# Kernel optimization log

Measured on AMD Instinct MI355X. Metric: run time of the kernel, lower is better.

Reference implementation:

```python
import jax, jax.numpy as jnp
import numpy as np

B, N, D, K = 16, 512, 64, 8  # batch, num_nodes, node_dim, num_edge_class


def setup_inputs() -> dict:
    key = jax.random.key(0)
    ks = jax.random.split(key, 6)
    return {
        "node_states": jax.random.normal(ks[0], (B, N, D), jnp.float32),
        "adjacency_in": jax.random.randint(ks[1], (B, N, N), 0, K + 1, jnp.int32),
        "distance": jax.random.normal(ks[2], (B, N, N), jnp.float32),  # declared but unused, as in source
        "matrices_in": jax.random.normal(ks[3], (K, D, D), jnp.float32) * 0.1,
        "matrices_out": jax.random.normal(ks[4], (K, D, D), jnp.float32) * 0.1,
        "message_bias": jax.random.normal(ks[5], (2 * D,), jnp.float32) * 0.1,
    }


def reference(node_states, adjacency_in, distance, matrices_in, matrices_out, message_bias):
    # node_states: [B, N, D]; adjacency_in: [B, N, N] int in [0, K]; 0 = no edge.
    node_dim = node_states.shape[-1]
    zeros = jnp.zeros((1, node_dim, node_dim), node_states.dtype)
    Min = jnp.concatenate([zeros, matrices_in], axis=0)    # [K+1, D, D]
    Mout = jnp.concatenate([zeros, matrices_out], axis=0)  # [K+1, D, D]
    # Transform every node state by every edge-type matrix once:
    # T[b, j, k, d] = sum_e M[k, d, e] * h[b, j, e]
    T_in = jnp.einsum('kde,bje->bjkd', Min, node_states)
    T_out = jnp.einsum('kde,bje->bjkd', Mout, node_states)
    # One-hot edge types: oh[b, i, j, k] = [adjacency_in[b, i, j] == k]
    oh = jax.nn.one_hot(adjacency_in, Min.shape[0], dtype=node_states.dtype)  # [B, N, N, K+1]
    # a_in_mul[b, i, d]  = sum_j M_in[adj[b,i,j]]  @ h[b, j]  (identical math to the
    # dense [B, N*D, N*D] block-matmul in the TF source, without materializing it)
    a_in_mul = jnp.einsum('bijk,bjkd->bid', oh, T_in)
    # a_out uses the transposed adjacency: adj_out[b,i,j] = adj[b,j,i]
    a_out_mul = jnp.einsum('bjik,bjkd->bid', oh, T_out)
    messages = jnp.concatenate([a_in_mul, a_out_mul], axis=-1) + message_bias
    return messages  # [B, N, 2*D]
```

## Files before the change

### kernel.cpp

```cpp
#include <hip/hip_runtime.h>
#include <hip/hip_fp16.h>

#define B_ 16
#define N_ 512
#define D_ 64
#define K_ 8

#define WSU_BYTES ((size_t)B_ * N_ * N_ * 4)
#define T_BYTES   ((size_t)B_ * N_ * (K_ + 1) * D_ * 2)
#define HBF_BYTES ((size_t)B_ * N_ * D_ * 2)
#define MBF_BYTES ((size_t)2 * K_ * D_ * D_ * 2)
#define TROWB 1152

typedef __attribute__((ext_vector_type(8))) short bf8_t;
typedef __attribute__((ext_vector_type(4))) float f4_t;

__device__ __forceinline__ unsigned short f2bf(float x) {
  union { float f; unsigned u; } c; c.f = x;
  unsigned r = c.u + 0x7FFFu + ((c.u >> 16) & 1u);
  return (unsigned short)(r >> 16);
}

__global__ __launch_bounds__(256) void conv_inputs(
    const float* __restrict__ h, const float* __restrict__ Min,
    const float* __restrict__ Mout,
    unsigned short* __restrict__ hbf, unsigned short* __restrict__ Mbf,
    unsigned short* __restrict__ Tin, unsigned short* __restrict__ Tout) {
  const int g = blockIdx.x * 256 + threadIdx.x;
  {
    const float4 v = ((const float4*)h)[g];
    ushort4 o; o.x = f2bf(v.x); o.y = f2bf(v.y); o.z = f2bf(v.z); o.w = f2bf(v.w);
    ((ushort4*)hbf)[g] = o;
  }
  if (g < 8192) {
    const float4 v = ((const float4*)Min)[g];
    ushort4 o; o.x = f2bf(v.x); o.y = f2bf(v.y); o.z = f2bf(v.z); o.w = f2bf(v.w);
    ((ushort4*)Mbf)[g] = o;
  } else if (g < 16384) {
    const int t = g - 8192;
    const float4 v = ((const float4*)Mout)[t];
    ushort4 o; o.x = f2bf(v.x); o.y = f2bf(v.y); o.z = f2bf(v.z); o.w = f2bf(v.w);
    ((ushort4*)Mbf)[8192 + t] = o;
  }
  {
    const int row = g >> 4, part = g & 15;
    const ushort4 z = make_ushort4(0, 0, 0, 0);
    ((ushort4*)(Tin  + (size_t)row * 576))[part] = z;
    ((ushort4*)(Tout + (size_t)row * 576))[part] = z;
  }
}

__global__ __launch_bounds__(256) void prep_adj(const int* __restrict__ adj,
                                                unsigned* __restrict__ wsu) {
  __shared__ int ta[64][65];
  __shared__ int tb[64][65];
  const int blk = blockIdx.x;
  const int xcd = blk & 7, rest = blk >> 3;
  const int b = xcd + 8 * (rest & 1);
  const int tile = rest >> 1;
  const int i0 = (tile >> 3) * 64, j0 = (tile & 7) * 64;
  const int lane = threadIdx.x & 63, w = threadIdx.x >> 6;
  const int* ab = adj + (size_t)b * N_ * N_;
#pragma unroll
  for (int r = w; r < 64; r += 4) {
    ta[r][lane] = ab[(size_t)(i0 + r) * N_ + j0 + lane];
    tb[r][lane] = ab[(size_t)(j0 + r) * N_ + i0 + lane];
  }
  __syncthreads();
  unsigned* wb = wsu + (size_t)b * N_ * N_;
#pragma unroll
  for (int r = w; r < 64; r += 4) {
    wb[(size_t)(i0 + r) * N_ + j0 + lane] =
        (unsigned)(ta[r][lane] << 7) | ((unsigned)tb[lane][r] << 23);
  }
}

__global__ __launch_bounds__(256) void build_T_mfma(
    const unsigned short* __restrict__ hbf,
    const unsigned short* __restrict__ Mbf,
    unsigned short* __restrict__ Tin,
    unsigned short* __restrict__ Tout) {
  const int blk = blockIdx.x;
  const int b   = (blk & 7) + 8 * ((blk >> 3) & 1);
  const int u   = blk >> 4;
  const int kdt = u >> 3;
  const int jt4 = u & 7;
  const int w = threadIdx.x >> 6, l = threadIdx.x & 63;
  const int j0  = (jt4 * 4 + w) * 16;
  const int kd0 = kdt * 64;
  const int r16 = l & 15, grp = l >> 4;

  const unsigned short* hr = hbf + ((size_t)(b * N_ + j0 + r16)) * 64 + grp * 8;
  bf8_t hfr[2];
  hfr[0] = *(const bf8_t*)(hr);
  hfr[1] = *(const bf8_t*)(hr + 32);

  const unsigned short* mr = Mbf + (size_t)(kd0 + r16) * 64 + grp * 8;

  f4_t acc[4];
#pragma unroll
  for (int fc = 0; fc < 4; ++fc) acc[fc] = (f4_t)(0.f);
#pragma unroll
  for (int fc = 0; fc < 4; ++fc) {
    const bf8_t a0 = *(const bf8_t*)(mr + (size_t)fc * 16 * 64);
    const bf8_t a1 = *(const bf8_t*)(mr + (size_t)fc * 16 * 64 + 32);
    acc[fc] = __builtin_amdgcn_mfma_f32_16x16x32_bf16(a0, hfr[0], acc[fc], 0, 0, 0);
    acc[fc] = __builtin_amdgcn_mfma_f32_16x16x32_bf16(a1, hfr[1], acc[fc], 0, 0, 0);
  }

  unsigned short* Tb = ((kd0 & 512) ? Tout : Tin) + (size_t)b * N_ * 576;
  const int kdl = kd0 & 511;
  const int j = j0 + r16;
  unsigned short* trow = Tb + (size_t)j * 576 + 64 + kdl + grp * 4;
#pragma unroll
  for (int fc = 0; fc < 4; ++fc) {
    const __half2 lo = __floats2half2_rn(acc[fc][0], acc[fc][1]);
    const __half2 hi = __floats2half2_rn(acc[fc][2], acc[fc][3]);
    uint2 pk;
    pk.x = *(const unsigned*)&lo;
    pk.y = *(const unsigned*)&hi;
    *(uint2*)(trow + fc * 16) = pk;
  }
}

__global__ __launch_bounds__(512) void gather_msg(
    const unsigned* __restrict__ wsu,
    const unsigned short* __restrict__ Tin,
    const float* __restrict__ bias,
    float* __restrict__ out) {
  __shared__ unsigned ed[16][512];
  const int blk = blockIdx.x;
  const int b  = (blk & 7) + 8 * ((blk >> 3) & 1);
  const int rb = blk >> 4;
  const int tid = threadIdx.x;
  const int w = tid >> 6, lane = tid & 63;
  const int half = lane >> 5, lane5 = lane & 31;
  const int dir = lane5 >> 4;
  const int dl  = lane5 & 15;
  const int row_l = w * 2 + half;

  {
    const int4* src = (const int4*)(wsu + ((size_t)(b * N_ + rb * 16)) * N_);
    int4* dst = (int4*)ed;
#pragma unroll
    for (int c = 0; c < 4; ++c) dst[c * 512 + tid] = src[c * 512 + tid];
  }
  __syncthreads();

  const unsigned shr_ = (unsigned)dir * 16u;
  const char* base = (const char*)Tin + (size_t)b * N_ * TROWB;
  unsigned vb = (unsigned)dir * (unsigned)T_BYTES + (unsigned)dl * 8u;
  const unsigned* edrow = &ed[row_l][0];

  float fa0 = 0.f, fa1 = 0.f, fa2 = 0.f, fa3 = 0.f;
  for (int jw = 0; jw < 8; ++jw) {
    __half2 a0 = __floats2half2_rn(0.f, 0.f);
    __half2 a1 = __floats2half2_rn(0.f, 0.f);
#pragma unroll 4
    for (int j4 = 0; j4 < 16; ++j4) {
      const uint4 ew = *(const uint4*)(edrow + jw * 64 + j4 * 4);
#pragma unroll
      for (int t = 0; t < 4; ++t) {
        const unsigned wvv = (t == 0) ? ew.x : (t == 1) ? ew.y : (t == 2) ? ew.z : ew.w;
        const unsigned off = (wvv >> shr_) & 0xFFFFu;
        const uint2 u = *(const uint2*)(base + (vb + off));
        a0 = __hadd2(a0, *(const __half2*)&u.x);
        a1 = __hadd2(a1, *(const __half2*)&u.y);
        vb += TROWB;
      }
    }
    const float2 f0 = __half22float2(a0);
    const float2 f1 = __half22float2(a1);
    fa0 += f0.x; fa1 += f0.y; fa2 += f1.x; fa3 += f1.y;
  }

  const int row = rb * 16 + row_l;
  const int d0 = dl * 4;
  float4 r;
  r.x = fa0 + bias[dir * 64 + d0];
  r.y = fa1 + bias[dir * 64 + d0 + 1];
  r.z = fa2 + bias[dir * 64 + d0 + 2];
  r.w = fa3 + bias[dir * 64 + d0 + 3];
  *(float4*)(out + ((size_t)b * N_ + row) * (2 * D_) + dir * 64 + d0) = r;
}

#define ACCUM(kv, bucket) switch (kv) { \
    case 1: (bucket)[0] += v_; break; case 2: (bucket)[1] += v_; break; \
    case 3: (bucket)[2] += v_; break; case 4: (bucket)[3] += v_; break; \
    case 5: (bucket)[4] += v_; break; case 6: (bucket)[5] += v_; break; \
    case 7: (bucket)[6] += v_; break; case 8: (bucket)[7] += v_; break; \
    default: break; }

__global__ __launch_bounds__(64) void ggnn_fallback(
    const float* __restrict__ h, const int* __restrict__ adj,
    const float* __restrict__ Min, const float* __restrict__ Mout,
    const float* __restrict__ bias, float* __restrict__ out) {
  const int blk = blockIdx.x;
  const int b  = blk / (N_ / 2);
  const int i0 = (blk % (N_ / 2)) * 2;
  const int d  = threadIdx.x;
  float s_in[2][K_], s_out[2][K_];
#pragma unroll
  for (int r = 0; r < 2; ++r)
#pragma unroll
    for (int k = 0; k < K_; ++k) { s_in[r][k] = 0.f; s_out[r][k] = 0.f; }
  const int* rowp0 = adj + (b * N_ + i0) * N_;
  const int* rowp1 = rowp0 + N_;
  const int* colp  = adj + b * N_ * N_ + i0;
  const float* hb  = h + b * N_ * D_ + d;
  for (int j0 = 0; j0 < N_; j0 += 8) {
    float hv[8]; int kr0[8], kr1[8], kc0[8], kc1[8];
#pragma unroll
    for (int m = 0; m < 8; ++m) {
      hv[m] = hb[(j0 + m) * D_];
      kr0[m] = rowp0[j0 + m]; kr1[m] = rowp1[j0 + m];
      kc0[m] = colp[(j0 + m) * N_]; kc1[m] = colp[(j0 + m) * N_ + 1];
    }
#pragma unroll
    for (int m = 0; m < 8; ++m) {
      const float v_ = hv[m];
      ACCUM(kr0[m], s_in[0]); ACCUM(kr1[m], s_in[1]);
      ACCUM(kc0[m], s_out[0]); ACCUM(kc1[m], s_out[1]);
    }
  }
  __shared__ float S[2][2][K_][D_];
#pragma unroll
  for (int r = 0; r < 2; ++r)
#pragma unroll
    for (int k = 0; k < K_; ++k) { S[r][0][k][d] = s_in[r][k]; S[r][1][k][d] = s_out[r][k]; }
  __syncthreads();
  float acc_in[2], acc_out[2];
#pragma unroll
  for (int r = 0; r < 2; ++r) { acc_in[r] = bias[d]; acc_out[r] = bias[D_ + d]; }
  for (int k = 0; k < K_; ++k) {
#pragma unroll
    for (int e0 = 0; e0 < D_; e0 += 4) {
      const float4 mi = *(const float4*)(Min  + (k * D_ + d) * D_ + e0);
      const float4 mo = *(const float4*)(Mout + (k * D_ + d) * D_ + e0);
#pragma unroll
      for (int r = 0; r < 2; ++r) {
        const float4 si = *(const float4*)(&S[r][0][k][e0]);
        const float4 so = *(const float4*)(&S[r][1][k][e0]);
        acc_in[r]  += mi.x * si.x + mi.y * si.y + mi.z * si.z + mi.w * si.w;
        acc_out[r] += mo.x * so.x + mo.y * so.y + mo.z * so.z + mo.w * so.w;
      }
    }
  }
#pragma unroll
  for (int r = 0; r < 2; ++r) {
    out[(b * N_ + i0 + r) * (2 * D_) + d]      = acc_in[r];
    out[(b * N_ + i0 + r) * (2 * D_) + D_ + d] = acc_out[r];
  }
}

extern "C" void kernel_launch(void* const* d_in, const int* in_sizes, int n_in,
                              void* d_out, int out_size, void* d_ws, size_t ws_size,
                              hipStream_t stream) {
  const float* h    = (const float*)d_in[0];
  const int*   adj  = (const int*)d_in[1];
  const float* Min  = (const float*)d_in[3];
  const float* Mout = (const float*)d_in[4];
  const float* bias = (const float*)d_in[5];
  float* out = (float*)d_out;

  if (ws_size < WSU_BYTES + 2 * T_BYTES + HBF_BYTES + MBF_BYTES) {
    hipLaunchKernelGGL(ggnn_fallback, dim3(B_ * N_ / 2), dim3(64), 0, stream,
                       h, adj, Min, Mout, bias, out);
    return;
  }
  unsigned*       wsu  = (unsigned*)d_ws;
  unsigned short* Tin  = (unsigned short*)((char*)d_ws + WSU_BYTES);
  unsigned short* Tout = (unsigned short*)((char*)d_ws + WSU_BYTES + T_BYTES);
  unsigned short* hbf  = (unsigned short*)((char*)d_ws + WSU_BYTES + 2 * T_BYTES);
  unsigned short* Mbf  = (unsigned short*)((char*)d_ws + WSU_BYTES + 2 * T_BYTES + HBF_BYTES);

  hipLaunchKernelGGL(conv_inputs,  dim3(512),  dim3(256), 0, stream,
                     h, Min, Mout, hbf, Mbf, Tin, Tout);
  hipLaunchKernelGGL(prep_adj,     dim3(1024), dim3(256), 0, stream, adj, wsu);
  hipLaunchKernelGGL(build_T_mfma, dim3(2048), dim3(256), 0, stream, hbf, Mbf, Tin, Tout);
  hipLaunchKernelGGL(gather_msg,   dim3(512),  dim3(512), 0, stream,
                     wsu, Tin, bias, out);
}
```

Before: 166.2 us.

## Fold bf16 input conversion into T build and split gather over j halves

Removes the separate conv_inputs kernel. build_T_mfma now converts fp32 h and M to bf16 in registers, and its kdt==0 blocks zero the k=0 slots of T_in and T_out. gather_msg now handles 8 rows per block instead of 16. The block's two wave groups each cover half of the j range, and their partial sums are combined through shared memory. This doubles the grid to 1024 blocks and fully unrolls the inner loop, so more of the GPU stays busy and one launch plus one global pass disappear. The cost is repeated fp32-to-bf16 conversion of M across many blocks and an extra shared-memory reduction with syncs.

```diff
diff --git a/kernel.cpp b/kernel.cpp
--- a/kernel.cpp
+++ b/kernel.cpp
@@ -8,9 +8,8 @@
 
 #define WSU_BYTES ((size_t)B_ * N_ * N_ * 4)
 #define T_BYTES   ((size_t)B_ * N_ * (K_ + 1) * D_ * 2)
-#define HBF_BYTES ((size_t)B_ * N_ * D_ * 2)
-#define MBF_BYTES ((size_t)2 * K_ * D_ * D_ * 2)
 #define TROWB 1152
+#define TOUT_OFF (T_BYTES / 2)
 
 typedef __attribute__((ext_vector_type(8))) short bf8_t;
 typedef __attribute__((ext_vector_type(4))) float f4_t;
@@ -21,33 +20,15 @@
   return (unsigned short)(r >> 16);
 }
 
-__global__ __launch_bounds__(256) void conv_inputs(
-    const float* __restrict__ h, const float* __restrict__ Min,
-    const float* __restrict__ Mout,
-    unsigned short* __restrict__ hbf, unsigned short* __restrict__ Mbf,
-    unsigned short* __restrict__ Tin, unsigned short* __restrict__ Tout) {
-  const int g = blockIdx.x * 256 + threadIdx.x;
-  {
-    const float4 v = ((const float4*)h)[g];
-    ushort4 o; o.x = f2bf(v.x); o.y = f2bf(v.y); o.z = f2bf(v.z); o.w = f2bf(v.w);
-    ((ushort4*)hbf)[g] = o;
-  }
-  if (g < 8192) {
-    const float4 v = ((const float4*)Min)[g];
-    ushort4 o; o.x = f2bf(v.x); o.y = f2bf(v.y); o.z = f2bf(v.z); o.w = f2bf(v.w);
-    ((ushort4*)Mbf)[g] = o;
-  } else if (g < 16384) {
-    const int t = g - 8192;
-    const float4 v = ((const float4*)Mout)[t];
-    ushort4 o; o.x = f2bf(v.x); o.y = f2bf(v.y); o.z = f2bf(v.z); o.w = f2bf(v.w);
-    ((ushort4*)Mbf)[8192 + t] = o;
-  }
-  {
-    const int row = g >> 4, part = g & 15;
-    const ushort4 z = make_ushort4(0, 0, 0, 0);
-    ((ushort4*)(Tin  + (size_t)row * 576))[part] = z;
-    ((ushort4*)(Tout + (size_t)row * 576))[part] = z;
-  }
+__device__ __forceinline__ bf8_t pack_bf8(const float* p) {
+  const float4 a = *(const float4*)p;
+  const float4 b = *(const float4*)(p + 4);
+  union { unsigned u[4]; bf8_t v; } r;
+  r.u[0] = (unsigned)f2bf(a.x) | ((unsigned)f2bf(a.y) << 16);
+  r.u[1] = (unsigned)f2bf(a.z) | ((unsigned)f2bf(a.w) << 16);
+  r.u[2] = (unsigned)f2bf(b.x) | ((unsigned)f2bf(b.y) << 16);
+  r.u[3] = (unsigned)f2bf(b.z) | ((unsigned)f2bf(b.w) << 16);
+  return r.v;
 }
 
 __global__ __launch_bounds__(256) void prep_adj(const int* __restrict__ adj,
@@ -76,10 +57,10 @@
 }
 
 __global__ __launch_bounds__(256) void build_T_mfma(
-    const unsigned short* __restrict__ hbf,
-    const unsigned short* __restrict__ Mbf,
-    unsigned short* __restrict__ Tin,
-    unsigned short* __restrict__ Tout) {
+    const float* __restrict__ h,
+    const float* __restrict__ Min,
+    const float* __restrict__ Mout,
+    unsigned short* __restrict__ Tin) {
   const int blk = blockIdx.x;
   const int b   = (blk & 7) + 8 * ((blk >> 3) & 1);
   const int u   = blk >> 4;
@@ -90,25 +71,26 @@
   const int kd0 = kdt * 64;
   const int r16 = l & 15, grp = l >> 4;
 
-  const unsigned short* hr = hbf + ((size_t)(b * N_ + j0 + r16)) * 64 + grp * 8;
+  const float* hrp = h + ((size_t)(b * N_ + j0 + r16)) * 64 + grp * 8;
   bf8_t hfr[2];
-  hfr[0] = *(const bf8_t*)(hr);
-  hfr[1] = *(const bf8_t*)(hr + 32);
-
-  const unsigned short* mr = Mbf + (size_t)(kd0 + r16) * 64 + grp * 8;
+  hfr[0] = pack_bf8(hrp);
+  hfr[1] = pack_bf8(hrp + 32);
+
+  const float* Mbase = (kd0 >= 512) ? Mout : Min;
+  const float* mrp = Mbase + (size_t)((kd0 & 511) + r16) * 64 + grp * 8;
 
   f4_t acc[4];
 #pragma unroll
   for (int fc = 0; fc < 4; ++fc) acc[fc] = (f4_t)(0.f);
 #pragma unroll
   for (int fc = 0; fc < 4; ++fc) {
-    const bf8_t a0 = *(const bf8_t*)(mr + (size_t)fc * 16 * 64);
-    const bf8_t a1 = *(const bf8_t*)(mr + (size_t)fc * 16 * 64 + 32);
+    const bf8_t a0 = pack_bf8(mrp + (size_t)fc * 16 * 64);
+    const bf8_t a1 = pack_bf8(mrp + (size_t)fc * 16 * 64 + 32);
     acc[fc] = __builtin_amdgcn_mfma_f32_16x16x32_bf16(a0, hfr[0], acc[fc], 0, 0, 0);
     acc[fc] = __builtin_amdgcn_mfma_f32_16x16x32_bf16(a1, hfr[1], acc[fc], 0, 0, 0);
   }
 
-  unsigned short* Tb = ((kd0 & 512) ? Tout : Tin) + (size_t)b * N_ * 576;
+  unsigned short* Tb = Tin + ((kd0 >= 512) ? TOUT_OFF : 0) + (size_t)b * N_ * 576;
   const int kdl = kd0 & 511;
   const int j = j0 + r16;
   unsigned short* trow = Tb + (size_t)j * 576 + 64 + kdl + grp * 4;
@@ -121,42 +103,53 @@
     pk.y = *(const unsigned*)&hi;
     *(uint2*)(trow + fc * 16) = pk;
   }
-}
-
-__global__ __launch_bounds__(512) void gather_msg(
+
+  if (kdt == 0) {
+    unsigned short* s0 = Tin + (size_t)b * N_ * 576 + (size_t)j * 576 + grp * 16;
+    const int4 z = make_int4(0, 0, 0, 0);
+    *(int4*)(s0)                 = z;
+    *(int4*)(s0 + 8)             = z;
+    *(int4*)(s0 + TOUT_OFF)      = z;
+    *(int4*)(s0 + TOUT_OFF + 8)  = z;
+  }
+}
+
+__global__ __launch_bounds__(512, 8) void gather_msg(
     const unsigned* __restrict__ wsu,
     const unsigned short* __restrict__ Tin,
     const float* __restrict__ bias,
     float* __restrict__ out) {
-  __shared__ unsigned ed[16][512];
+  __shared__ unsigned ed[8 * 512];
   const int blk = blockIdx.x;
   const int b  = (blk & 7) + 8 * ((blk >> 3) & 1);
   const int rb = blk >> 4;
   const int tid = threadIdx.x;
   const int w = tid >> 6, lane = tid & 63;
+  const int wq = w & 3, jh = w >> 2;
   const int half = lane >> 5, lane5 = lane & 31;
   const int dir = lane5 >> 4;
   const int dl  = lane5 & 15;
-  const int row_l = w * 2 + half;
+  const int row_l = wq * 2 + half;
 
   {
-    const int4* src = (const int4*)(wsu + ((size_t)(b * N_ + rb * 16)) * N_);
+    const int4* src = (const int4*)(wsu + ((size_t)(b * N_ + rb * 8)) * N_);
     int4* dst = (int4*)ed;
-#pragma unroll
-    for (int c = 0; c < 4; ++c) dst[c * 512 + tid] = src[c * 512 + tid];
-  }
-  __syncthreads();
-
+    dst[tid]       = src[tid];
+    dst[tid + 512] = src[tid + 512];
+  }
+  __syncthreads();
+
+  const unsigned* edrow = ed + row_l * 512 + jh * 256;
   const unsigned shr_ = (unsigned)dir * 16u;
   const char* base = (const char*)Tin + (size_t)b * N_ * TROWB;
-  unsigned vb = (unsigned)dir * (unsigned)T_BYTES + (unsigned)dl * 8u;
-  const unsigned* edrow = &ed[row_l][0];
+  unsigned vb = (unsigned)jh * 256u * (unsigned)TROWB +
+                (unsigned)dir * (unsigned)T_BYTES + (unsigned)dl * 8u;
 
   float fa0 = 0.f, fa1 = 0.f, fa2 = 0.f, fa3 = 0.f;
-  for (int jw = 0; jw < 8; ++jw) {
+  for (int jw = 0; jw < 4; ++jw) {
     __half2 a0 = __floats2half2_rn(0.f, 0.f);
     __half2 a1 = __floats2half2_rn(0.f, 0.f);
-#pragma unroll 4
+#pragma unroll
     for (int j4 = 0; j4 < 16; ++j4) {
       const uint4 ew = *(const uint4*)(edrow + jw * 64 + j4 * 4);
 #pragma unroll
@@ -174,14 +167,21 @@
     fa0 += f0.x; fa1 += f0.y; fa2 += f1.x; fa3 += f1.y;
   }
 
-  const int row = rb * 16 + row_l;
-  const int d0 = dl * 4;
-  float4 r;
-  r.x = fa0 + bias[dir * 64 + d0];
-  r.y = fa1 + bias[dir * 64 + d0 + 1];
-  r.z = fa2 + bias[dir * 64 + d0 + 2];
-  r.w = fa3 + bias[dir * 64 + d0 + 3];
-  *(float4*)(out + ((size_t)b * N_ + row) * (2 * D_) + dir * 64 + d0) = r;
+  __syncthreads();
+  float4* pbuf = (float4*)ed;
+  if (jh == 1) pbuf[wq * 64 + lane] = make_float4(fa0, fa1, fa2, fa3);
+  __syncthreads();
+  if (jh == 0) {
+    const float4 p = pbuf[wq * 64 + lane];
+    const int row = rb * 8 + row_l;
+    const int d0 = dl * 4;
+    float4 r;
+    r.x = fa0 + p.x + bias[dir * 64 + d0];
+    r.y = fa1 + p.y + bias[dir * 64 + d0 + 1];
+    r.z = fa2 + p.z + bias[dir * 64 + d0 + 2];
+    r.w = fa3 + p.w + bias[dir * 64 + d0 + 3];
+    *(float4*)(out + ((size_t)b * N_ + row) * (2 * D_) + dir * 64 + d0) = r;
+  }
 }
 
 #define ACCUM(kv, bucket) switch (kv) { \
@@ -263,21 +263,15 @@
   const float* bias = (const float*)d_in[5];
   float* out = (float*)d_out;
 
-  if (ws_size < WSU_BYTES + 2 * T_BYTES + HBF_BYTES + MBF_BYTES) {
+  if (ws_size < WSU_BYTES + 2 * T_BYTES) {
     hipLaunchKernelGGL(ggnn_fallback, dim3(B_ * N_ / 2), dim3(64), 0, stream,
                        h, adj, Min, Mout, bias, out);
     return;
   }
-  unsigned*       wsu  = (unsigned*)d_ws;
-  unsigned short* Tin  = (unsigned short*)((char*)d_ws + WSU_BYTES);
-  unsigned short* Tout = (unsigned short*)((char*)d_ws + WSU_BYTES + T_BYTES);
-  unsigned short* hbf  = (unsigned short*)((char*)d_ws + WSU_BYTES + 2 * T_BYTES);
-  unsigned short* Mbf  = (unsigned short*)((char*)d_ws + WSU_BYTES + 2 * T_BYTES + HBF_BYTES);
-
-  hipLaunchKernelGGL(conv_inputs,  dim3(512),  dim3(256), 0, stream,
-                     h, Min, Mout, hbf, Mbf, Tin, Tout);
+  unsigned*       wsu = (unsigned*)d_ws;
+  unsigned short* Tin = (unsigned short*)((char*)d_ws + WSU_BYTES);
+
   hipLaunchKernelGGL(prep_adj,     dim3(1024), dim3(256), 0, stream, adj, wsu);
-  hipLaunchKernelGGL(build_T_mfma, dim3(2048), dim3(256), 0, stream, hbf, Mbf, Tin, Tout);
-  hipLaunchKernelGGL(gather_msg,   dim3(512),  dim3(512), 0, stream,
-                     wsu, Tin, bias, out);
-}
+  hipLaunchKernelGGL(build_T_mfma, dim3(2048), dim3(256), 0, stream, h, Min, Mout, Tin);
+  hipLaunchKernelGGL(gather_msg,   dim3(1024), dim3(512), 0, stream, wsu, Tin, bias, out);
+}
```

New measurement: 171.9 us. 3.5% more time.
